# Kernel optimization log

Hardware: AMD Instinct MI355X
Metric: run time of the kernel (lower is better)

Reference implementation:

```python
import jax, jax.numpy as jnp
import numpy as np
from jax import lax

B, P, GRID, NP = 16, 220, 4, 16
DIM, DEPTH, HEADS, DH, MLP, NC = 512, 6, 8, 64, 2048, 1000
EPS = 1e-5
SCALE = DH ** -0.5
FLAT = 64 * 16 * 16  # per-patch CNN output [64,16,16] flattened (c,p1,p2 order)


def setup_inputs() -> dict:
    key = jax.random.key(0)
    ks = iter(jax.random.split(key, 40))
    def n(shape, std):
        return jax.random.normal(next(ks), shape, dtype=jnp.float32) * std
    return {
        "img": jax.random.normal(next(ks), (B, 1, GRID * P, GRID * P), dtype=jnp.float32),
        "conv1_w": n((32, 1, 7, 7), (2.0 / 49) ** 0.5),
        "conv2_w": n((64, 32, 7, 7), (2.0 / (32 * 49)) ** 0.5),
        "conv3_w": n((64, 64, 7, 7), (2.0 / (64 * 49)) ** 0.5),
        "flat_w": n((FLAT, DIM), FLAT ** -0.5),
        "flat_b": jnp.zeros((DIM,), jnp.float32),
        "cls_token": n((1, 1, DIM), 0.02),
        "pos_emb": n((1, NP + 1, DIM), 0.02),
        "ln1_g": jnp.ones((DEPTH, DIM), jnp.float32),
        "ln1_b": jnp.zeros((DEPTH, DIM), jnp.float32),
        "qkv_w": n((DEPTH, DIM, 3 * HEADS * DH), DIM ** -0.5),
        "out_w": n((DEPTH, HEADS * DH, DIM), (HEADS * DH) ** -0.5),
        "out_b": jnp.zeros((DEPTH, DIM), jnp.float32),
        "ln2_g": jnp.ones((DEPTH, DIM), jnp.float32),
        "ln2_b": jnp.zeros((DEPTH, DIM), jnp.float32),
        "ff1_w": n((DEPTH, DIM, MLP), DIM ** -0.5),
        "ff1_b": jnp.zeros((DEPTH, MLP), jnp.float32),
        "ff2_w": n((DEPTH, MLP, DIM), MLP ** -0.5),
        "ff2_b": jnp.zeros((DEPTH, DIM), jnp.float32),
        "head_ln_g": jnp.ones((DIM,), jnp.float32),
        "head_ln_b": jnp.zeros((DIM,), jnp.float32),
        "head_w": n((DIM, NC), DIM ** -0.5),
        "head_b": jnp.zeros((NC,), jnp.float32),
    }


def _ln(x, g, b):
    m = jnp.mean(x, axis=-1, keepdims=True)
    v = jnp.mean(jnp.square(x - m), axis=-1, keepdims=True)
    return (x - m) * lax.rsqrt(v + EPS) * g + b


def _cnn(x, w1, w2, w3):
    def block(h, w):
        h = lax.conv_general_dilated(h, w, (2, 2), 'VALID',
                                     dimension_numbers=('NCHW', 'OIHW', 'NCHW'))
        h = jax.nn.relu(h)
        # MaxPool2d(kernel=7, stride=1, padding=1)
        return lax.reduce_window(h, -jnp.inf, lax.max, (1, 1, 7, 7), (1, 1, 1, 1),
                                 ((0, 0), (0, 0), (1, 1), (1, 1)))
    return block(block(block(x, w1), w2), w3)


def _forward(img, conv1_w, conv2_w, conv3_w, flat_w, flat_b, cls_token, pos_emb,
             ln1_g, ln1_b, qkv_w, out_w, out_b, ln2_g, ln2_b,
             ff1_w, ff1_b, ff2_w, ff2_b, head_ln_g, head_ln_b, head_w, head_b):
    # b c (h p1) (w p2) -> (b h w) 1 p1 p2 ; all patches batched through the CNN at once
    patches = img.reshape(B, 1, GRID, P, GRID, P).transpose(0, 2, 4, 3, 1, 5)
    patches = patches.reshape(B * NP, 1, P, P)
    feat = _cnn(patches, conv1_w, conv2_w, conv3_w).reshape(B, NP, FLAT)  # [B,NP,64*16*16]
    x = feat @ flat_w + flat_b                                            # [B,NP,DIM]
    x = jnp.concatenate([jnp.broadcast_to(cls_token, (B, 1, DIM)), x], axis=1) + pos_emb
    N = NP + 1

    def layer(x, p):
        g1, b1, qw, ow, ob, g2, b2, w1, fb1, w2, fb2 = p
        h = _ln(x, g1, b1)
        q, k, v = jnp.split(h @ qw, 3, axis=-1)
        def heads(t):
            return t.reshape(B, N, HEADS, DH).transpose(0, 2, 1, 3)  # b h n d
        q, k, v = heads(q), heads(k), heads(v)
        attn = jax.nn.softmax(jnp.einsum('bhqd,bhkd->bhqk', q, k) * SCALE, axis=-1)
        o = jnp.einsum('bhqk,bhkd->bhqd', attn, v).transpose(0, 2, 1, 3).reshape(B, N, HEADS * DH)
        x = x + o @ ow + ob
        h2 = _ln(x, g2, b2)
        x = x + jax.nn.gelu(h2 @ w1 + fb1, approximate=False) @ w2 + fb2
        return x, None

    x, _ = lax.scan(layer, x, (ln1_g, ln1_b, qkv_w, out_w, out_b,
                               ln2_g, ln2_b, ff1_w, ff1_b, ff2_w, ff2_b))
    cls = _ln(x[:, 0], head_ln_g, head_ln_b)
    return cls @ head_w + head_b  # [B, NC]


def reference(img, conv1_w, conv2_w, conv3_w, flat_w, flat_b, cls_token, pos_emb,
              ln1_g, ln1_b, qkv_w, out_w, out_b, ln2_g, ln2_b,
              ff1_w, ff1_b, ff2_w, ff2_b, head_ln_g, head_ln_b, head_w, head_b):
    return _forward(img, conv1_w, conv2_w, conv3_w, flat_w, flat_b, cls_token, pos_emb,
                    ln1_g, ln1_b, qkv_w, out_w, out_b, ln2_g, ln2_b,
                    ff1_w, ff1_b, ff2_w, ff2_b, head_ln_g, head_ln_b, head_w, head_b)
```

## Files before the change

### kernel.cpp

```cpp
#include <hip/hip_runtime.h>
#include <hip/hip_bf16.h>


typedef __hip_bfloat16 bf16;
typedef __attribute__((ext_vector_type(8))) short short8;
typedef __attribute__((ext_vector_type(4))) float floatx4;

#define CHUNK 64

union U8 { int4 v; unsigned short s[8]; };
__device__ inline void umax8(U8& a, const U8& b){
  #pragma unroll
  for (int j = 0; j < 8; j++) a.s[j] = (a.s[j] > b.s[j]) ? a.s[j] : b.s[j];
}
union U4 { uint2 v; unsigned short s[4]; };
__device__ inline void umax4(U4& a, const U4& b){
  #pragma unroll
  for (int j = 0; j < 4; j++) a.s[j] = (a.s[j] > b.s[j]) ? a.s[j] : b.s[j];
}

__global__ __launch_bounds__(256) void prep_w2(const float* __restrict__ w,
                                               bf16* __restrict__ w2b)
{
  int idx = blockIdx.x*256 + threadIdx.x;
  if (idx >= 49*64*32) return;
  int ic = idx & 31; int t = idx >> 5; int oc = t & 63; int kk = t >> 6;
  int ky = kk/7, kx = kk - ky*7;
  w2b[idx] = __float2bfloat16(w[((oc*32+ic)*7+ky)*7+kx]);
}

__global__ __launch_bounds__(256) void prep_w3(const float* __restrict__ w,
                                               bf16* __restrict__ w3b)
{
  int idx = blockIdx.x*256 + threadIdx.x;
  if (idx >= 49*2*64*32) return;
  int ic_l = idx & 31; int t = idx >> 5; int oc = t & 63; int t2 = t >> 6;
  int kx = t2 % 7; int t3 = t2 / 7; int kc = t3 & 1; int ky = t3 >> 1;
  w3b[idx] = __float2bfloat16(w[((oc*64 + kc*32 + ic_l)*7+ky)*7+kx]);
}

__global__ __launch_bounds__(256) void prep_pack(
    const float* __restrict__ src, bf16* __restrict__ dst,
    int K8, int N, int total)
{
  int idx = blockIdx.x*256 + threadIdx.x;
  if (idx >= total) return;
  int n = idx % N; int t = idx / N; int k8 = t % K8; int l = t / K8;
  const float* s = src + ((size_t)l*K8*8 + (size_t)k8*8)*N + n;
  union { bf16 h[8]; int4 v; } pk;
  #pragma unroll
  for (int j = 0; j < 8; j++) pk.h[j] = __float2bfloat16(s[(size_t)j*N]);
  *(int4*)(dst + (((size_t)l*K8 + k8)*N + n)*8) = pk.v;
}

__global__ __launch_bounds__(256) void prep_pack_flat(
    const float* __restrict__ src, bf16* __restrict__ hi, bf16* __restrict__ lo)
{
  int idx = blockIdx.x*256 + threadIdx.x;
  if (idx >= 2048*512) return;
  int n = idx & 511; int k8 = idx >> 9;
  const float* s = src + (size_t)k8*8*512 + n;
  union { bf16 h[8]; int4 v; } ph, pl;
  #pragma unroll
  for (int j = 0; j < 8; j++){
    float w = s[(size_t)j*512];
    bf16 h = __float2bfloat16(w);
    ph.h[j] = h;
    pl.h[j] = __float2bfloat16(w - __bfloat162float(h));
  }
  size_t o = (size_t)idx*8;
  *(int4*)(hi + o) = ph.v;
  *(int4*)(lo + o) = pl.v;
}

__global__ __launch_bounds__(256) void k1a_conv1(
    const float* __restrict__ img, const float* __restrict__ w,
    bf16* __restrict__ cbuf, int n_base)
{
  __shared__ __align__(16) float in_s[15*224];
  __shared__ float w_s[32*58];
  const int band = blockIdx.x;
  const int n = blockIdx.y;
  const int ng = n_base + n;
  const int r0 = band*5;
  const int ir0 = 2*r0;
  const int b = ng>>4, gh = (ng>>2)&3, gw = ng&3;
  const float* ibase = img + b*774400 + (gh*220)*880 + gw*220;

  for (int idx = threadIdx.x; idx < 15*56; idx += 256){
    int r = idx/56, cq = idx - r*56; int c = cq*4;
    int gr = ir0 + r;
    float4 v = (c < 220 && gr < 220) ? *(const float4*)(ibase + gr*880 + c)
                                     : make_float4(0.f,0.f,0.f,0.f);
    *(float4*)&in_s[r*224 + c] = v;
  }
  for (int idx = threadIdx.x; idx < 32*56; idx += 256){
    int oc = idx/56, k = idx - oc*56; int ky = k>>3, kx = k&7;
    w_s[oc*58 + k] = (kx < 7) ? w[oc*49 + ky*7 + kx] : 0.f;
  }
  __syncthreads();

  const int grp = threadIdx.x & 7;
  const int sp  = threadIdx.x >> 3;
  const int cgc = (sp < 26) ? sp : 26;
  const int nrows = (107 - r0 < 5) ? (107 - r0) : 5;

  float acc[5][4][4] = {};
  #pragma unroll 1
  for (int ky = 0; ky < 7; ky++){
    float wk[4][7];
    #pragma unroll
    for (int oc = 0; oc < 4; oc++)
      #pragma unroll
      for (int kx = 0; kx < 7; kx++)
        wk[oc][kx] = w_s[(grp*4+oc)*58 + ky*8 + kx];
    #pragma unroll
    for (int i = 0; i < 5; i++){
      if (i < nrows){
        const float* ip = &in_s[(2*i+ky)*224 + 8*cgc];
        float iv[13];
        *(float4*)&iv[0] = *(const float4*)ip;
        *(float4*)&iv[4] = *(const float4*)(ip+4);
        *(float4*)&iv[8] = *(const float4*)(ip+8);
        iv[12] = ip[12];
        #pragma unroll
        for (int oc = 0; oc < 4; oc++)
          #pragma unroll
          for (int kx = 0; kx < 7; kx++)
            #pragma unroll
            for (int j = 0; j < 4; j++)
              acc[i][oc][j] += iv[2*j+kx]*wk[oc][kx];
      }
    }
  }

  #pragma unroll
  for (int i = 0; i < 5; i++){
    if (i < nrows){
      int y = r0 + i;
      #pragma unroll
      for (int j = 0; j < 4; j++){
        int col = 4*sp + j;
        if (col < 107){
          union { unsigned short s[4]; uint2 u; } pk;
          #pragma unroll
          for (int oc = 0; oc < 4; oc++){
            bf16 hv = __float2bfloat16(fmaxf(acc[i][oc][j], 0.f));
            pk.s[oc] = *(unsigned short*)&hv;
          }
          *(uint2*)(cbuf + (((size_t)(n*8+grp)*107 + y)*107 + col)*4) = pk.u;
        }
      }
    }
  }
}

__global__ __launch_bounds__(256) void k1b_pool1(
    const bf16* __restrict__ cbuf, bf16* __restrict__ pool1, int n_pool_base)
{
  __shared__ uint2 in4[19*107];
  __shared__ uint2 ht4[19*103];
  const int s = blockIdx.x, g = blockIdx.y, n = blockIdx.z;
  const int p0 = s*13;
  const int PR = (103 - p0 < 13) ? (103 - p0) : 13;
  const int NR = PR + 6;
  const uint2* src = (const uint2*)cbuf + (size_t)(n*8+g)*107*107;

  for (int t = threadIdx.x; t < NR*107; t += 256){
    int r = t/107, c = t - r*107;
    int gr = p0 - 1 + r;
    gr = (gr < 0) ? 0 : ((gr > 106) ? 106 : gr);
    in4[t] = src[gr*107 + c];
  }
  __syncthreads();
  for (int t = threadIdx.x; t < NR*103; t += 256){
    int r = t/103, c = t - r*103;
    U4 m; m.v = in4[r*107 + ((c > 0) ? c-1 : 0)];
    #pragma unroll
    for (int d = 0; d < 6; d++){
      U4 v; v.v = in4[r*107 + ((c+d < 106) ? c+d : 106)];
      umax4(m, v);
    }
    ht4[r*103 + c] = m.v;
  }
  __syncthreads();
  uint2* dst = (uint2*)pool1;
  const size_t plane = ((size_t)(n_pool_base + n)*4 + (g>>1))*10609;
  const int h = g & 1;
  for (int t = threadIdx.x; t < PR*103; t += 256){
    int pr = t/103, c = t - pr*103;
    U4 m; m.v = ht4[pr*103 + c];
    #pragma unroll
    for (int d = 1; d < 7; d++){
      U4 v; v.v = ht4[(pr+d)*103 + c];
      umax4(m, v);
    }
    dst[(plane + (size_t)(p0+pr)*103 + c)*2 + h] = m.v;
  }
}

__global__ __launch_bounds__(256) void k2_conv2(
    const bf16* __restrict__ pool1,
    const bf16* __restrict__ w2b,
    bf16* __restrict__ conv2out)
{
  __shared__ __align__(16) bf16 in_s[7*2*52*36];
  const int n = blockIdx.y, pb = blockIdx.x;
  const int wv = threadIdx.x >> 6, lane = threadIdx.x & 63;
  const int li = lane & 15, lg = lane >> 4;
  const int p0 = pb*256;
  const int y0 = p0/49;

  int pyv[4], pxv[4]; bool pmask[4];
  #pragma unroll
  for (int t = 0; t < 4; t++){
    int p = p0 + wv*64 + t*16 + li;
    pmask[t] = (p <= 2400);
    int pc = min(p, 2400);
    int yy = pc/49, xx = pc - yy*49;
    pyv[t] = yy; pxv[t] = xx;
  }
  floatx4 acc[4][4];
  #pragma unroll
  for (int a = 0; a < 4; a++)
    #pragma unroll
    for (int t = 0; t < 4; t++) acc[a][t] = (floatx4){0.f,0.f,0.f,0.f};

  const unsigned short* pbase = (const unsigned short*)pool1;

  auto stage_rows = [&](int e0, int cnt, int par){
    for (int idx = threadIdx.x; idx < cnt*103*4; idx += 256){
      int q = idx & 3; int t2 = idx >> 2; int ri = t2/103; int c = t2 - ri*103;
      int e = e0 + ri;
      int slot = e % 7;
      int gr = min(2*e + par, 102);
      *(int4*)&in_s[((slot*2 + (c&1))*52 + (c>>1))*36 + q*8] =
        *(const int4*)(pbase + (((size_t)n*4 + q)*10609 + (size_t)gr*103 + c)*8);
    }
  };

  const int kyseq[7] = {0,2,4,6,1,3,5};
  #pragma unroll 1
  for (int ks = 0; ks < 7; ks++){
    int ky = kyseq[ks];
    int kyh = ky >> 1, par = ky & 1;
    __syncthreads();
    if (ks == 0 || ks == 4) stage_rows(y0, 7, par);
    else                    stage_rows(y0 + 6 + kyh, 1, par);
    __syncthreads();
    int poff[4];
    #pragma unroll
    for (int t = 0; t < 4; t++){
      int e = pyv[t] + kyh;
      int slot = e % 7;
      poff[t] = (slot*2*52 + pxv[t])*36;
    }
    #pragma unroll
    for (int kx = 0; kx < 7; kx++){
      short8 a[4];
      const bf16* wp = w2b + (ky*7+kx)*64*32;
      #pragma unroll
      for (int ot = 0; ot < 4; ot++)
        a[ot] = *(const short8*)(wp + (ot*16 + li)*32 + lg*8);
      int koff = ((kx&1)*52 + (kx>>1))*36 + lg*8;
      #pragma unroll
      for (int t = 0; t < 4; t++){
        short8 bfr = *(const short8*)(&in_s[poff[t] + koff]);
        #pragma unroll
        for (int ot = 0; ot < 4; ot++)
          acc[ot][t] = __builtin_amdgcn_mfma_f32_16x16x32_bf16(a[ot], bfr, acc[ot][t], 0, 0, 0);
      }
    }
  }
  #pragma unroll
  for (int t = 0; t < 4; t++){
    if (!pmask[t]) continue;
    bf16* dst = conv2out + (((long)n*49 + pyv[t])*49 + pxv[t])*64 + lg*4;
    #pragma unroll
    for (int ot = 0; ot < 4; ot++){
      union { bf16 h[4]; uint2 u; } pk;
      #pragma unroll
      for (int v = 0; v < 4; v++)
        pk.h[v] = __float2bfloat16(fmaxf(acc[ot][t][v], 0.f));
      *(uint2*)(dst + ot*16) = pk.u;
    }
  }
}

__global__ __launch_bounds__(256) void k3a_hmax(
    const bf16* __restrict__ cin, bf16* __restrict__ tmp)
{
  int idx = blockIdx.x*256 + threadIdx.x;
  int cg = idx & 7; int t = idx >> 3; int x = t % 45; int t2 = t / 45;
  int y = t2 % 49; int n = t2 / 49;
  const int4* row = (const int4*)(cin + ((long)(n*49 + y)*49)*64) + cg;
  U8 m; m.v = make_int4(0,0,0,0);
  int lo = max(x-1, 0), hi = min(x+5, 48);
  for (int cx = lo; cx <= hi; cx++){ U8 v; v.v = row[cx*8]; umax8(m, v); }
  *((int4*)(tmp + ((long)(n*49 + y)*45 + x)*64) + cg) = m.v;
}

__global__ __launch_bounds__(256) void k3b_vmax(
    const bf16* __restrict__ tmp, bf16* __restrict__ pout, int n_base)
{
  int idx = blockIdx.x*256 + threadIdx.x;
  int cg = idx & 7; int t = idx >> 3; int x = t % 45; int t2 = t / 45;
  int y = t2 % 45; int n = t2 / 45;
  U8 m; m.v = make_int4(0,0,0,0);
  int lo = max(y-1, 0), hi = min(y+5, 48);
  for (int cy = lo; cy <= hi; cy++){
    U8 v; v.v = *((const int4*)(tmp + ((long)(n*49 + cy)*45 + x)*64) + cg);
    umax8(m, v);
  }
  *((int4*)(pout + (long)(n_base+n)*129600 + (y*45 + x)*64) + cg) = m.v;
}

__global__ __launch_bounds__(256) void k4_conv3(
    const bf16* __restrict__ pool2,
    const bf16* __restrict__ w3b,
    bf16* __restrict__ conv3out)
{
  __shared__ __align__(16) bf16 in_s[10*2*24*40];
  const int n = blockIdx.y, pb = blockIdx.x;
  const int wv = threadIdx.x >> 6, lane = threadIdx.x & 63;
  const int li = lane & 15, lg = lane >> 4;
  const int y0 = pb*10;

  int pyv[4], pxv[4]; bool pmask[4];
  #pragma unroll
  for (int t = 0; t < 4; t++){
    int pl = wv*64 + t*16 + li;
    pmask[t] = (pl < 200);
    int p = pb*200 + min(pl, 199);
    int yy = p/20, xx = p - yy*20;
    pyv[t] = yy; pxv[t] = xx;
  }
  floatx4 acc[4][4];
  #pragma unroll
  for (int a = 0; a < 4; a++)
    #pragma unroll
    for (int t = 0; t < 4; t++) acc[a][t] = (floatx4){0.f,0.f,0.f,0.f};

  auto stage_rows = [&](int e0, int cnt, int par, int kc){
    for (int idx = threadIdx.x; idx < cnt*45*4; idx += 256){
      int q = idx & 3; int t2 = idx >> 2; int ri = t2/45; int c = t2 - ri*45;
      int e = e0 + ri;
      int slot = e % 10;
      int gr = 2*e + par;
      *(int4*)&in_s[((slot*2 + (c&1))*24 + (c>>1))*40 + q*8] =
        *(const int4*)(pool2 + (((long)n*45 + gr)*45 + c)*64 + kc*32 + q*8);
    }
  };

  const int kyseq[7] = {0,2,4,6,1,3,5};
  #pragma unroll 1
  for (int kc = 0; kc < 2; kc++){
    #pragma unroll 1
    for (int ks = 0; ks < 7; ks++){
      int ky = kyseq[ks];
      int kyh = ky >> 1, par = ky & 1;
      __syncthreads();
      if (ks == 0 || ks == 4) stage_rows(y0 + kyh, 10, par, kc);
      else                    stage_rows(y0 + 9 + kyh, 1, par, kc);
      __syncthreads();
      int poff[4];
      #pragma unroll
      for (int t = 0; t < 4; t++){
        int e = pyv[t] + kyh;
        int slot = e % 10;
        poff[t] = (slot*2*24 + pxv[t])*40;
      }
      #pragma unroll
      for (int kx = 0; kx < 7; kx++){
        short8 a[4];
        const bf16* wp = w3b + ((ky*2+kc)*7 + kx)*64*32;
        #pragma unroll
        for (int ot = 0; ot < 4; ot++)
          a[ot] = *(const short8*)(wp + (ot*16 + li)*32 + lg*8);
        int koff = ((kx&1)*24 + (kx>>1))*40 + lg*8;
        #pragma unroll
        for (int t = 0; t < 4; t++){
          short8 bfr = *(const short8*)(&in_s[poff[t] + koff]);
          #pragma unroll
          for (int ot = 0; ot < 4; ot++)
            acc[ot][t] = __builtin_amdgcn_mfma_f32_16x16x32_bf16(a[ot], bfr, acc[ot][t], 0, 0, 0);
        }
      }
    }
  }
  #pragma unroll
  for (int t = 0; t < 4; t++){
    if (!pmask[t]) continue;
    bf16* dst = conv3out + (((long)n*20 + pyv[t])*20 + pxv[t])*64 + lg*4;
    #pragma unroll
    for (int ot = 0; ot < 4; ot++){
      union { bf16 h[4]; uint2 u; } pk;
      #pragma unroll
      for (int v = 0; v < 4; v++)
        pk.h[v] = __float2bfloat16(fmaxf(acc[ot][t][v], 0.f));
      *(uint2*)(dst + ot*16) = pk.u;
    }
  }
}

__global__ __launch_bounds__(256) void k5_pool3(
    const bf16* __restrict__ cin, bf16* __restrict__ feat)
{
  __shared__ int4 in_p[3200];
  __shared__ int4 ht[2560];
  const int n = blockIdx.x;
  const int4* src = (const int4*)(cin + (long)n*25600);
  for (int i = threadIdx.x; i < 3200; i += 256) in_p[i] = src[i];
  __syncthreads();
  for (int i = threadIdx.x; i < 2560; i += 256){
    int cg = i & 7; int t = i >> 3; int x = t & 15; int y = t >> 4;
    U8 m; m.v = make_int4(0,0,0,0);
    int lo = max(x-1, 0), hi = min(x+5, 19);
    for (int cx = lo; cx <= hi; cx++){ U8 v; v.v = in_p[(y*20+cx)*8 + cg]; umax8(m, v); }
    ht[(y*16+x)*8 + cg] = m.v;
  }
  __syncthreads();
  unsigned short* dst = (unsigned short*)(feat + (long)n*16384);
  for (int i = threadIdx.x; i < 2048; i += 256){
    int px = i & 15; int py = (i >> 4) & 15; int cg = i >> 8;
    U8 m; m.v = make_int4(0,0,0,0);
    int lo = max(py-1, 0), hi = min(py+5, 19);
    for (int cy = lo; cy <= hi; cy++){ U8 v; v.v = ht[(cy*16+px)*8 + cg]; umax8(m, v); }
    #pragma unroll
    for (int j = 0; j < 8; j++)
      dst[(cg*8+j)*256 + py*16 + px] = m.s[j];
  }
}

__global__ __launch_bounds__(256) void k6_init_x(
    const float* __restrict__ cls, const float* __restrict__ pos,
    const float* __restrict__ flat_b, float* __restrict__ x)
{
  int idx = blockIdx.x*256 + threadIdx.x;
  int d = idx & 511; int row = idx >> 9;
  int tt = row % 17;
  x[idx] = (tt == 0) ? (cls[d] + pos[d]) : (flat_b[d] + pos[tt*512 + d]);
}

__global__ __launch_bounds__(256) void k6_flat_mfma(
    const bf16* __restrict__ feat, const bf16* __restrict__ Whi,
    const bf16* __restrict__ Wlo, float* __restrict__ x)
{
  const int wv = threadIdx.x >> 6, lane = threadIdx.x & 63;
  const int li = lane & 15, lg = lane >> 4;
  const int m0 = blockIdx.x*64;
  const int nb = blockIdx.y*64 + wv*16;
  const int kb = blockIdx.z*512;
  floatx4 acc[4];
  #pragma unroll
  for (int t = 0; t < 4; t++) acc[t] = (floatx4){0.f,0.f,0.f,0.f};

  const bf16* abase = feat + (size_t)(m0+li)*16384 + kb + lg*8;
  for (int k0 = 0; k0 < 512; k0 += 32){
    short8 a0 = *(const short8*)(abase + k0);
    short8 a1 = *(const short8*)(abase + (size_t)16*16384 + k0);
    short8 a2 = *(const short8*)(abase + (size_t)32*16384 + k0);
    short8 a3 = *(const short8*)(abase + (size_t)48*16384 + k0);
    size_t wo = ((size_t)((kb + k0) >> 3) + lg)*512 + nb + li;
    short8 bh = *(const short8*)(Whi + wo*8);
    short8 bl = *(const short8*)(Wlo + wo*8);
    acc[0] = __builtin_amdgcn_mfma_f32_16x16x32_bf16(a0, bh, acc[0], 0, 0, 0);
    acc[1] = __builtin_amdgcn_mfma_f32_16x16x32_bf16(a1, bh, acc[1], 0, 0, 0);
    acc[2] = __builtin_amdgcn_mfma_f32_16x16x32_bf16(a2, bh, acc[2], 0, 0, 0);
    acc[3] = __builtin_amdgcn_mfma_f32_16x16x32_bf16(a3, bh, acc[3], 0, 0, 0);
    acc[0] = __builtin_amdgcn_mfma_f32_16x16x32_bf16(a0, bl, acc[0], 0, 0, 0);
    acc[1] = __builtin_amdgcn_mfma_f32_16x16x32_bf16(a1, bl, acc[1], 0, 0, 0);
    acc[2] = __builtin_amdgcn_mfma_f32_16x16x32_bf16(a2, bl, acc[2], 0, 0, 0);
    acc[3] = __builtin_amdgcn_mfma_f32_16x16x32_bf16(a3, bl, acc[3], 0, 0, 0);
  }
  int col = nb + li;
  #pragma unroll
  for (int t = 0; t < 4; t++){
    #pragma unroll
    for (int v = 0; v < 4; v++){
      int m = m0 + t*16 + lg*4 + v;
      int row = (m>>4)*17 + 1 + (m&15);
      atomicAdd(&x[row*512 + col], acc[t][v]);
    }
  }
}

__global__ __launch_bounds__(256) void ln_kernel(
    const float* __restrict__ in, const float* __restrict__ g,
    const float* __restrict__ b, float* __restrict__ out,
    int in_stride, int out_stride)
{
  int row = blockIdx.x;
  const float* p = in + (long)row*in_stride;
  float v0 = p[threadIdx.x], v1 = p[threadIdx.x+256];
  __shared__ float red[4]; __shared__ float stat;
  float s = v0+v1;
  #pragma unroll
  for (int o = 32; o >= 1; o >>= 1) s += __shfl_down(s, o);
  int lane = threadIdx.x & 63, wv = threadIdx.x >> 6;
  if (lane == 0) red[wv] = s;
  __syncthreads();
  if (threadIdx.x == 0) stat = (red[0]+red[1]+red[2]+red[3])*(1.0f/512.0f);
  __syncthreads();
  float m = stat;
  float d0 = v0-m, d1 = v1-m;
  float q = d0*d0 + d1*d1;
  #pragma unroll
  for (int o = 32; o >= 1; o >>= 1) q += __shfl_down(q, o);
  __syncthreads();
  if (lane == 0) red[wv] = q;
  __syncthreads();
  if (threadIdx.x == 0) stat = rsqrtf((red[0]+red[1]+red[2]+red[3])*(1.0f/512.0f) + 1e-5f);
  __syncthreads();
  float rstd = stat;
  out[(long)row*out_stride + threadIdx.x]     = d0*rstd*g[threadIdx.x]     + b[threadIdx.x];
  out[(long)row*out_stride + threadIdx.x+256] = d1*rstd*g[threadIdx.x+256] + b[threadIdx.x+256];
}

__global__ __launch_bounds__(256) void ln_bf16(
    const float* __restrict__ in, const float* __restrict__ g,
    const float* __restrict__ b, bf16* __restrict__ out)
{
  int row = blockIdx.x;
  const float* p = in + (long)row*512;
  float v0 = p[threadIdx.x], v1 = p[threadIdx.x+256];
  __shared__ float red[4]; __shared__ float stat;
  float s = v0+v1;
  #pragma unroll
  for (int o = 32; o >= 1; o >>= 1) s += __shfl_down(s, o);
  int lane = threadIdx.x & 63, wv = threadIdx.x >> 6;
  if (lane == 0) red[wv] = s;
  __syncthreads();
  if (threadIdx.x == 0) stat = (red[0]+red[1]+red[2]+red[3])*(1.0f/512.0f);
  __syncthreads();
  float m = stat;
  float d0 = v0-m, d1 = v1-m;
  float q = d0*d0 + d1*d1;
  #pragma unroll
  for (int o = 32; o >= 1; o >>= 1) q += __shfl_down(q, o);
  __syncthreads();
  if (lane == 0) red[wv] = q;
  __syncthreads();
  if (threadIdx.x == 0) stat = rsqrtf((red[0]+red[1]+red[2]+red[3])*(1.0f/512.0f) + 1e-5f);
  __syncthreads();
  float rstd = stat;
  out[(long)row*512 + threadIdx.x]     = __float2bfloat16(d0*rstd*g[threadIdx.x]     + b[threadIdx.x]);
  out[(long)row*512 + threadIdx.x+256] = __float2bfloat16(d1*rstd*g[threadIdx.x+256] + b[threadIdx.x+256]);
}

template<int NT>
__global__ __launch_bounds__(256) void tail_gemm(
    const bf16* __restrict__ A, const bf16* __restrict__ Wp,
    const float* __restrict__ bias, const float* res,
    float* outf, bf16* outb, int N, int K, int dogelu)
{
  const int wv = threadIdx.x >> 6, lane = threadIdx.x & 63;
  const int li = lane & 15, lg = lane >> 4;
  const int m0 = blockIdx.x * 16;
  const int nb = blockIdx.y * (64*NT) + wv * (16*NT);
  floatx4 acc[NT];
  #pragma unroll
  for (int t = 0; t < NT; t++) acc[t] = (floatx4){0.f,0.f,0.f,0.f};
  const bf16* arow = A + (size_t)(m0+li)*K + lg*8;
  for (int k0 = 0; k0 < K; k0 += 32){
    short8 a = *(const short8*)(arow + k0);
    const bf16* wrow = Wp + ((size_t)((k0>>3) + lg) * N + nb + li) * 8;
    #pragma unroll
    for (int t = 0; t < NT; t++){
      short8 bfr = *(const short8*)(wrow + t*128);
      acc[t] = __builtin_amdgcn_mfma_f32_16x16x32_bf16(a, bfr, acc[t], 0, 0, 0);
    }
  }
  #pragma unroll
  for (int t = 0; t < NT; t++){
    int col = nb + t*16 + li;
    #pragma unroll
    for (int v = 0; v < 4; v++){
      int row = m0 + lg*4 + v;
      float val = acc[t][v];
      if (bias) val += bias[col];
      if (dogelu) val = 0.5f*val*(1.0f + erff(val*0.70710678118654752f));
      if (res) val += res[(size_t)row*N + col];
      if (outf) outf[(size_t)row*N + col] = val;
      else      outb[(size_t)row*N + col] = __float2bfloat16(val);
    }
  }
}

__global__ __launch_bounds__(256) void gemm_rows(
    const float* __restrict__ A, const float* __restrict__ W,
    const float* __restrict__ bias, const float* __restrict__ res,
    float* __restrict__ out, int M, int N, int K, int dogelu)
{
  __shared__ float A_s[16][33];
  __shared__ __align__(16) float W_s[32][68];
  const int m0 = blockIdx.x*16, n0 = blockIdx.y*64;
  const int r = threadIdx.x>>4, c0 = (threadIdx.x&15)*4;
  float acc[4] = {};
  for (int k0 = 0; k0 < K; k0 += 32){
    __syncthreads();
    for (int i = 0; i < 2; i++){ int id = threadIdx.x + i*256; int rr = id>>5, kk = id&31;
      A_s[rr][kk] = (m0+rr < M) ? A[(long)(m0+rr)*K + k0+kk] : 0.f; }
    for (int i = 0; i < 8; i++){ int id = threadIdx.x + i*256; int kk = id>>6, c = id&63;
      W_s[kk][c] = (n0+c < N) ? W[(long)(k0+kk)*N + n0+c] : 0.f; }
    __syncthreads();
    #pragma unroll
    for (int kk = 0; kk < 32; kk++){
      float a = A_s[r][kk];
      float4 w4 = *(const float4*)&W_s[kk][c0];
      acc[0]+=a*w4.x; acc[1]+=a*w4.y; acc[2]+=a*w4.z; acc[3]+=a*w4.w;
    }
  }
  if (m0+r < M){
    int row = m0+r;
    for (int j = 0; j < 4; j++){
      int c = n0+c0+j;
      if (c < N){
        float v = acc[j];
        if (bias) v += bias[c];
        if (dogelu) v = 0.5f*v*(1.0f + erff(v*0.70710678118654752f));
        if (res) v += res[(long)row*N + c];
        out[(long)row*N + c] = v;
      }
    }
  }
}

__global__ __launch_bounds__(128) void attn_kernel(
    const float* __restrict__ qkv, bf16* __restrict__ obuf)
{
  const int b = blockIdx.x >> 3, h = blockIdx.x & 7;
  __shared__ float q_s[17][65], k_s[17][65], v_s[17][65], s_s[17][18];
  for (int idx = threadIdx.x; idx < 17*64; idx += 128){
    int i = idx>>6, d = idx&63;
    const float* base = qkv + (long)(b*17+i)*1536 + h*64 + d;
    q_s[i][d] = base[0]; k_s[i][d] = base[512]; v_s[i][d] = base[1024];
  }
  __syncthreads();
  for (int idx = threadIdx.x; idx < 289; idx += 128){
    int i = idx/17, j = idx - i*17;
    float s = 0.f;
    for (int d = 0; d < 64; d++) s += q_s[i][d]*k_s[j][d];
    s_s[i][j] = s*0.125f;
  }
  __syncthreads();
  if (threadIdx.x < 17){
    int i = threadIdx.x;
    float m = -1e30f;
    for (int j = 0; j < 17; j++) m = fmaxf(m, s_s[i][j]);
    float sum = 0.f;
    for (int j = 0; j < 17; j++){ float e = expf(s_s[i][j]-m); s_s[i][j] = e; sum += e; }
    float inv = 1.0f/sum;
    for (int j = 0; j < 17; j++) s_s[i][j] *= inv;
  }
  __syncthreads();
  for (int idx = threadIdx.x; idx < 17*64; idx += 128){
    int i = idx>>6, d = idx&63;
    float o = 0.f;
    for (int j = 0; j < 17; j++) o += s_s[i][j]*v_s[j][d];
    obuf[(long)(b*17+i)*512 + h*64 + d] = __float2bfloat16(o);
  }
}

extern "C" void kernel_launch(void* const* d_in, const int* in_sizes, int n_in,
                              void* d_out, int out_size, void* d_ws, size_t ws_size,
                              hipStream_t stream) {
  const float* img      = (const float*)d_in[0];
  const float* conv1_w  = (const float*)d_in[1];
  const float* conv2_w  = (const float*)d_in[2];
  const float* conv3_w  = (const float*)d_in[3];
  const float* flat_w   = (const float*)d_in[4];
  const float* flat_b   = (const float*)d_in[5];
  const float* cls_tok  = (const float*)d_in[6];
  const float* pos_emb  = (const float*)d_in[7];
  const float* ln1_g    = (const float*)d_in[8];
  const float* ln1_b    = (const float*)d_in[9];
  const float* qkv_w    = (const float*)d_in[10];
  const float* out_w    = (const float*)d_in[11];
  const float* out_b    = (const float*)d_in[12];
  const float* ln2_g    = (const float*)d_in[13];
  const float* ln2_b    = (const float*)d_in[14];
  const float* ff1_w    = (const float*)d_in[15];
  const float* ff1_b    = (const float*)d_in[16];
  const float* ff2_w    = (const float*)d_in[17];
  const float* ff2_b    = (const float*)d_in[18];
  const float* hln_g    = (const float*)d_in[19];
  const float* hln_b    = (const float*)d_in[20];
  const float* head_w   = (const float*)d_in[21];
  const float* head_b   = (const float*)d_in[22];

  char* ws = (char*)d_ws;
  size_t off = 0;
  auto alloc = [&](size_t bytes) -> void* {
    void* p = ws + off; off += (bytes + 255) & ~(size_t)255; return p;
  };
  bf16* pool1    = (bf16*)alloc((size_t)CHUNK*8*103*103*4*2);
  bf16* conv2out = (bf16*)alloc((size_t)CHUNK*49*49*64*2);
  bf16* pool2    = (bf16*)alloc((size_t)256*45*45*64*2);
  bf16* feat     = (bf16*)alloc((size_t)256*16384*2);
  bf16* w2b      = (bf16*)alloc((size_t)49*64*32*2);
  bf16* w3b      = (bf16*)alloc((size_t)49*2*64*32*2);
  float* x       = (float*)alloc((size_t)139264*4);
  bf16*  hb      = (bf16*)alloc((size_t)139264*2);
  float* qkvb    = (float*)alloc((size_t)417792*4);
  bf16*  obufb   = (bf16*)alloc((size_t)139264*2);
  bf16*  ffbufb  = (bf16*)alloc((size_t)557056*2);
  float* hcls    = (float*)alloc((size_t)8192*4);
  bf16* tmp3     = pool1;
  bf16* conv3out = pool1;
  bf16* qkvp  = pool1;
  bf16* outwp = qkvp  + (size_t)6*512*1536;
  bf16* ff1p  = outwp + (size_t)6*512*512;
  bf16* ff2p  = ff1p  + (size_t)6*512*2048;
  bf16* fwhi  = conv2out;
  bf16* fwlo  = pool2;

  const size_t cb_per_n = (size_t)8*107*107*4*2;
  int SUB; bf16* cbuf;
  if (ws_size >= off + 64*cb_per_n)      { SUB = 64; cbuf = (bf16*)alloc(64*cb_per_n); }
  else if (ws_size >= off + 32*cb_per_n) { SUB = 32; cbuf = (bf16*)alloc(32*cb_per_n); }
  else { SUB = 16; cbuf = conv2out; }
  (void)in_sizes; (void)n_in; (void)out_size;

  prep_w2<<<392, 256, 0, stream>>>(conv2_w, w2b);
  prep_w3<<<784, 256, 0, stream>>>(conv3_w, w3b);

  for (int cb = 0; cb < 256; cb += CHUNK){
    for (int sb = 0; sb < CHUNK; sb += SUB){
      k1a_conv1<<<dim3(22, SUB), 256, 0, stream>>>(img, conv1_w, cbuf, cb + sb);
      k1b_pool1<<<dim3(8, 8, SUB), 256, 0, stream>>>(cbuf, pool1, sb);
    }
    k2_conv2     <<<dim3(10,CHUNK), 256, 0, stream>>>(pool1, w2b, conv2out);
    k3a_hmax     <<<(CHUNK*49*45*8)/256, 256, 0, stream>>>(conv2out, tmp3);
    k3b_vmax     <<<(CHUNK*45*45*8)/256, 256, 0, stream>>>(tmp3, pool2, cb);
  }
  k4_conv3<<<dim3(2,256), 256, 0, stream>>>(pool2, w3b, conv3out);
  k5_pool3<<<256, 256, 0, stream>>>(conv3out, feat);

  prep_pack_flat<<<4096, 256, 0, stream>>>(flat_w, fwhi, fwlo);
  prep_pack<<<(6*64*1536+255)/256, 256, 0, stream>>>(qkv_w, qkvp, 64, 1536, 6*64*1536);
  prep_pack<<<(6*64*512 +255)/256, 256, 0, stream>>>(out_w, outwp, 64, 512,  6*64*512);
  prep_pack<<<(6*64*2048+255)/256, 256, 0, stream>>>(ff1_w, ff1p, 64, 2048, 6*64*2048);
  prep_pack<<<(6*256*512+255)/256, 256, 0, stream>>>(ff2_w, ff2p, 256, 512, 6*256*512);

  k6_init_x    <<<544,          256, 0, stream>>>(cls_tok, pos_emb, flat_b, x);
  k6_flat_mfma <<<dim3(4,8,32), 256, 0, stream>>>(feat, fwhi, fwlo, x);

  for (int l = 0; l < 6; l++){
    ln_bf16<<<272, 256, 0, stream>>>(x, ln1_g + l*512, ln1_b + l*512, hb);
    tail_gemm<4><<<dim3(17,6), 256, 0, stream>>>(hb, qkvp + (size_t)l*786432,
                                                 nullptr, nullptr, qkvb, nullptr, 1536, 512, 0);
    attn_kernel<<<128, 128, 0, stream>>>(qkvb, obufb);
    tail_gemm<1><<<dim3(17,8), 256, 0, stream>>>(obufb, outwp + (size_t)l*262144,
                                                 out_b + l*512, x, x, nullptr, 512, 512, 0);
    ln_bf16<<<272, 256, 0, stream>>>(x, ln2_g + l*512, ln2_b + l*512, hb);
    tail_gemm<4><<<dim3(17,8), 256, 0, stream>>>(hb, ff1p + (size_t)l*1048576,
                                                 ff1_b + l*2048, nullptr, nullptr, ffbufb, 2048, 512, 1);
    tail_gemm<1><<<dim3(17,8), 256, 0, stream>>>(ffbufb, ff2p + (size_t)l*1048576,
                                                 ff2_b + l*512, x, x, nullptr, 512, 2048, 0);
  }

  ln_kernel<<<16, 256, 0, stream>>>(x, hln_g, hln_b, hcls, 17*512, 512);
  gemm_rows<<<dim3(1,16), 256, 0, stream>>>(hcls, head_w, head_b, nullptr,
                                            (float*)d_out, 16, 1000, 512, 0);
}
```

Measured before the change: 1.548 ms.

## Stage all conv2 input rows per parity at once to cut barriers

The conv2 kernel previously used a 7-slot ring buffer in shared memory, restaging one input row per kernel-row step with two barriers each time. It now loads 10 rows (even parity) or 9 rows (odd parity) into a larger shared buffer in one pass, then runs all kernel rows of that parity without further synchronisation. This removes five barrier pairs and the modulo slot arithmetic. In exchange, shared memory rises from about 52 KB to about 75 KB per block, which may lower occupancy, and a single large staging step exposes more load latency up front.

```diff
diff --git a/kernel.cpp b/kernel.cpp
--- a/kernel.cpp
+++ b/kernel.cpp
@@ -204,14 +204,14 @@
     const bf16* __restrict__ w2b,
     bf16* __restrict__ conv2out)
 {
-  __shared__ __align__(16) bf16 in_s[7*2*52*36];
+  __shared__ __align__(16) bf16 in_s[10*2*52*36];
   const int n = blockIdx.y, pb = blockIdx.x;
   const int wv = threadIdx.x >> 6, lane = threadIdx.x & 63;
   const int li = lane & 15, lg = lane >> 4;
   const int p0 = pb*256;
   const int y0 = p0/49;
 
-  int pyv[4], pxv[4]; bool pmask[4];
+  int pyv[4], pxv[4], pbase_[4]; bool pmask[4];
   #pragma unroll
   for (int t = 0; t < 4; t++){
     int p = p0 + wv*64 + t*16 + li;
@@ -219,6 +219,7 @@
     int pc = min(p, 2400);
     int yy = pc/49, xx = pc - yy*49;
     pyv[t] = yy; pxv[t] = xx;
+    pbase_[t] = ((yy - y0)*104 + xx)*36;
   }
   floatx4 acc[4][4];
   #pragma unroll
@@ -228,33 +229,19 @@
 
   const unsigned short* pbase = (const unsigned short*)pool1;
 
-  auto stage_rows = [&](int e0, int cnt, int par){
+  auto stage_rows = [&](int cnt, int par){
     for (int idx = threadIdx.x; idx < cnt*103*4; idx += 256){
       int q = idx & 3; int t2 = idx >> 2; int ri = t2/103; int c = t2 - ri*103;
-      int e = e0 + ri;
-      int slot = e % 7;
-      int gr = min(2*e + par, 102);
-      *(int4*)&in_s[((slot*2 + (c&1))*52 + (c>>1))*36 + q*8] =
+      int gr = min(2*(y0+ri) + par, 102);
+      *(int4*)&in_s[((ri*2 + (c&1))*52 + (c>>1))*36 + q*8] =
         *(const int4*)(pbase + (((size_t)n*4 + q)*10609 + (size_t)gr*103 + c)*8);
     }
   };
 
-  const int kyseq[7] = {0,2,4,6,1,3,5};
-  #pragma unroll 1
-  for (int ks = 0; ks < 7; ks++){
-    int ky = kyseq[ks];
-    int kyh = ky >> 1, par = ky & 1;
-    __syncthreads();
-    if (ks == 0 || ks == 4) stage_rows(y0, 7, par);
-    else                    stage_rows(y0 + 6 + kyh, 1, par);
-    __syncthreads();
+  auto compute_phase = [&](int ky, int kyh){
     int poff[4];
     #pragma unroll
-    for (int t = 0; t < 4; t++){
-      int e = pyv[t] + kyh;
-      int slot = e % 7;
-      poff[t] = (slot*2*52 + pxv[t])*36;
-    }
+    for (int t = 0; t < 4; t++) poff[t] = pbase_[t] + kyh*3744;
     #pragma unroll
     for (int kx = 0; kx < 7; kx++){
       short8 a[4];
@@ -271,7 +258,18 @@
           acc[ot][t] = __builtin_amdgcn_mfma_f32_16x16x32_bf16(a[ot], bfr, acc[ot][t], 0, 0, 0);
       }
     }
-  }
+  };
+
+  stage_rows(10, 0);
+  __syncthreads();
+  #pragma unroll 1
+  for (int kyh = 0; kyh < 4; kyh++) compute_phase(2*kyh, kyh);
+  __syncthreads();
+  stage_rows(9, 1);
+  __syncthreads();
+  #pragma unroll 1
+  for (int kyh = 0; kyh < 3; kyh++) compute_phase(2*kyh+1, kyh);
+
   #pragma unroll
   for (int t = 0; t < 4; t++){
     if (!pmask[t]) continue;
```

New measurement: 1.535 ms. Within noise of the previous version (-0.8%).
